# Optimization experiments

Hardware: AMD Instinct MI355X
Metric: run time of the kernel (lower is better)

Reference implementation:

```python
import jax, jax.numpy as jnp
import numpy as np

D_MODEL = 1024
NUM_HEADS = 16
D_K = D_MODEL // NUM_HEADS
LOCAL_WINDOW = 3
STRIDE = 4


def strided_mask(seq_len):
    # position i attends to j iff j <= i and (i-j <= local_window or (i-j) % stride == 0)
    i = jnp.arange(seq_len)[:, None]
    j = jnp.arange(seq_len)[None, :]
    d = i - j
    return (d >= 0) & ((d <= LOCAL_WINDOW) | (d % STRIDE == 0))


def setup_inputs() -> dict:
    key = jax.random.key(0)
    ks = jax.random.split(key, 11)
    B, S, D = 4, 1024, D_MODEL
    s = 1.0 / np.sqrt(D)
    inp = {
        "Q": jax.random.normal(ks[0], (B, S, D), jnp.float32),
        "K": jax.random.normal(ks[1], (B, S, D), jnp.float32),
        "V": jax.random.normal(ks[2], (B, S, D), jnp.float32),
        "Wq": jax.random.normal(ks[3], (D, D), jnp.float32) * s,
        "bq": jnp.zeros((D,), jnp.float32),
        "Wk": jax.random.normal(ks[4], (D, D), jnp.float32) * s,
        "bk": jnp.zeros((D,), jnp.float32),
        "Wv": jax.random.normal(ks[5], (D, D), jnp.float32) * s,
        "bv": jnp.zeros((D,), jnp.float32),
        "Wo": jax.random.normal(ks[6], (D, D), jnp.float32) * s,
        "bo": jnp.zeros((D,), jnp.float32),
    }
    return inp


def reference(Q, K, V, Wq, bq, Wk, bk, Wv, bv, Wo, bo):
    B, S, D = Q.shape
    H, dk = NUM_HEADS, D_K

    def split(x):  # [B,S,D] -> [B,H,S,dk]
        return x.reshape(B, S, H, dk).transpose(0, 2, 1, 3)

    q = split(Q @ Wq + bq)
    k = split(K @ Wk + bk)
    v = split(V @ Wv + bv)

    scores = jnp.einsum("bhsd,bhtd->bhst", q, k) / jnp.sqrt(
        jnp.asarray(dk, jnp.float32))
    m = strided_mask(S)[None, None]  # [1,1,S,S]
    scores = jnp.where(m, scores, -1e9)
    attn = jax.nn.softmax(scores, axis=-1)
    out = jnp.einsum("bhst,bhtd->bhsd", attn, v)
    out = out.transpose(0, 2, 1, 3).reshape(B, S, D)  # combine heads
    return out @ Wo + bo
```

## Files before the change

### kernel.cpp

```cpp
#include <hip/hip_runtime.h>

typedef _Float16 f16;
typedef __attribute__((ext_vector_type(8))) _Float16 f16x8;
typedef __attribute__((ext_vector_type(4))) _Float16 f16x4;
typedef __attribute__((ext_vector_type(4))) float f32x4;

#define MFMA16(a, b, c) __builtin_amdgcn_mfma_f32_16x16x32_f16((a), (b), (c), 0, 0, 0)

__device__ __forceinline__ void gld_lds16(const void* g, void* l) {
  __builtin_amdgcn_global_load_lds(
      (__attribute__((address_space(1))) void*)const_cast<void*>(g),
      (__attribute__((address_space(3))) void*)l, 16, 0, 0);
}

__device__ __forceinline__ f16x8 ld8(const f16* p) { return *(const f16x8*)p; }

__global__ __launch_bounds__(256) void prep_kernel(
    const float* __restrict__ Q, const float* __restrict__ K, const float* __restrict__ V,
    const float* __restrict__ Wq, const float* __restrict__ Wk,
    const float* __restrict__ Wv, const float* __restrict__ Wo,
    f16* __restrict__ Xq, f16* __restrict__ Xk, f16* __restrict__ Xv,
    f16* __restrict__ Tq, f16* __restrict__ Tk, f16* __restrict__ Tv, f16* __restrict__ To) {
  const int bx = blockIdx.x;
  __shared__ float tile[64][65];
  if (bx < 6144) {
    const int z = bx >> 11, blk = bx & 2047;
    const float* src = z == 0 ? Q : (z == 1 ? K : V);
    f16* dst = z == 0 ? Xq : (z == 1 ? Xk : Xv);
    size_t i = ((size_t)blk * 256 + threadIdx.x) * 8;
    float4 a = *(const float4*)(src + i);
    float4 b = *(const float4*)(src + i + 4);
    f16x8 h;
    h[0] = (f16)a.x; h[1] = (f16)a.y; h[2] = (f16)a.z; h[3] = (f16)a.w;
    h[4] = (f16)b.x; h[5] = (f16)b.y; h[6] = (f16)b.z; h[7] = (f16)b.w;
    *(f16x8*)(dst + i) = h;
  } else {
    const int idx = bx - 6144;
    const int z = idx >> 8, xy = idx & 255;
    const float* W = z == 0 ? Wq : (z == 1 ? Wk : (z == 2 ? Wv : Wo));
    f16* T = z == 0 ? Tq : (z == 1 ? Tk : (z == 2 ? Tv : To));
    const int k0 = (xy & 15) * 64, n0 = (xy >> 4) * 64;
    const int tx = threadIdx.x & 63, ty = threadIdx.x >> 6;
#pragma unroll
    for (int rr = 0; rr < 16; ++rr) {
      int r = rr * 4 + ty;
      tile[r][tx] = W[(size_t)(k0 + r) * 1024 + n0 + tx];
    }
    __syncthreads();
#pragma unroll
    for (int rr = 0; rr < 16; ++rr) {
      int nn = rr * 4 + ty;
      T[(size_t)(n0 + nn) * 1024 + k0 + tx] = (f16)tile[tx][nn];
    }
  }
}

__global__ __launch_bounds__(256) void gemm_qkv_kernel(
    const f16* __restrict__ Xq, const f16* __restrict__ Xk, const f16* __restrict__ Xv,
    const f16* __restrict__ Bq, const f16* __restrict__ Bk, const f16* __restrict__ Bv,
    const float* __restrict__ bq, const float* __restrict__ bk, const float* __restrict__ bv,
    f16* __restrict__ qh, f16* __restrict__ kh,
    f16* __restrict__ vh, f16* __restrict__ vtg) {
  const int z = blockIdx.z;
  const f16* A = z == 0 ? Xq : (z == 1 ? Xk : Xv);
  const f16* Bt = z == 0 ? Bq : (z == 1 ? Bk : Bv);
  const float* bias = z == 0 ? bq : (z == 1 ? bk : bv);

  __shared__ alignas(16) f16 lA[128 * 32];
  __shared__ alignas(16) f16 lB[128 * 32];

  const int t = threadIdx.x;
  const int w = t >> 6, lane = t & 63, quad = lane >> 4, l15 = lane & 15;
  const int wm = w >> 1, wn = w & 1;
  const int mbase = blockIdx.x * 128;
  const int nbase = blockIdx.y * 128;

  const f32x4 zero4 = {0.f, 0.f, 0.f, 0.f};
  f32x4 acc[4][4];
#pragma unroll
  for (int mi = 0; mi < 4; ++mi)
#pragma unroll
    for (int ni = 0; ni < 4; ++ni) acc[mi][ni] = zero4;

  const int r = t >> 2;
  const int koff = (t & 3) * 8;

  for (int k0 = 0; k0 < 1024; k0 += 32) {
    __syncthreads();
    gld_lds16(A + (size_t)(mbase + r) * 1024 + k0 + koff, (char*)lA + w * 1024);
    gld_lds16(A + (size_t)(mbase + 64 + r) * 1024 + k0 + koff, (char*)lA + 4096 + w * 1024);
    gld_lds16(Bt + (size_t)(nbase + r) * 1024 + k0 + koff, (char*)lB + w * 1024);
    gld_lds16(Bt + (size_t)(nbase + 64 + r) * 1024 + k0 + koff, (char*)lB + 4096 + w * 1024);
    __syncthreads();

    f16x8 af[4], bf[4];
#pragma unroll
    for (int mi = 0; mi < 4; ++mi)
      af[mi] = ld8(&lA[(wm * 64 + mi * 16 + l15) * 32 + quad * 8]);
#pragma unroll
    for (int ni = 0; ni < 4; ++ni)
      bf[ni] = ld8(&lB[(wn * 64 + ni * 16 + l15) * 32 + quad * 8]);
#pragma unroll
    for (int mi = 0; mi < 4; ++mi)
#pragma unroll
      for (int ni = 0; ni < 4; ++ni)
        acc[mi][ni] = MFMA16(af[mi], bf[ni], acc[mi][ni]);
  }

#pragma unroll
  for (int mi = 0; mi < 4; ++mi) {
#pragma unroll
    for (int ni = 0; ni < 4; ++ni) {
#pragma unroll
      for (int rg = 0; rg < 4; ++rg) {
        const int row = mbase + wm * 64 + mi * 16 + quad * 4 + rg;
        const int col = nbase + wn * 64 + ni * 16 + l15;
        const float v = acc[mi][ni][rg] + bias[col];
        const int bh = (row >> 10) * 16 + (col >> 6);
        const int s = row & 1023, d = col & 63;
        const f16 hv = (f16)v;
        if (z == 0) {
          qh[(size_t)bh * 65536 + s * 64 + d] = hv;
        } else if (z == 1) {
          kh[(size_t)bh * 65536 + s * 64 + d] = hv;
        } else {
          vh[(size_t)bh * 65536 + s * 64 + d] = hv;
          const int rr = s & 3, n = s >> 2, wi = n & 63;
          vtg[(size_t)bh * 65536 + (size_t)rr * 16384 + (size_t)d * 256 +
              (n & ~63) + ((wi & 15) << 2) + (wi >> 4)] = hv;
        }
      }
    }
  }
}

__global__ __launch_bounds__(256) void gemm_out_kernel(
    const f16* __restrict__ A, const f16* __restrict__ Bt,
    const float* __restrict__ bias, float* __restrict__ Cf) {
  __shared__ alignas(16) f16 lA[64 * 32];
  __shared__ alignas(16) f16 lB[128 * 32];

  const int t = threadIdx.x;
  const int w = t >> 6, lane = t & 63, quad = lane >> 4, l15 = lane & 15;
  const int wm = w >> 1, wn = w & 1;
  const int mbase = blockIdx.x * 64;
  const int nbase = blockIdx.y * 128;

  const f32x4 zero4 = {0.f, 0.f, 0.f, 0.f};
  f32x4 acc[2][4];
#pragma unroll
  for (int mi = 0; mi < 2; ++mi)
#pragma unroll
    for (int ni = 0; ni < 4; ++ni) acc[mi][ni] = zero4;

  const int r = t >> 2;
  const int koff = (t & 3) * 8;

  for (int k0 = 0; k0 < 1024; k0 += 32) {
    __syncthreads();
    gld_lds16(A + (size_t)(mbase + r) * 1024 + k0 + koff, (char*)lA + w * 1024);
    gld_lds16(Bt + (size_t)(nbase + r) * 1024 + k0 + koff, (char*)lB + w * 1024);
    gld_lds16(Bt + (size_t)(nbase + 64 + r) * 1024 + k0 + koff, (char*)lB + 4096 + w * 1024);
    __syncthreads();

    f16x8 af[2], bf[4];
#pragma unroll
    for (int mi = 0; mi < 2; ++mi)
      af[mi] = ld8(&lA[(wm * 32 + mi * 16 + l15) * 32 + quad * 8]);
#pragma unroll
    for (int ni = 0; ni < 4; ++ni)
      bf[ni] = ld8(&lB[(wn * 64 + ni * 16 + l15) * 32 + quad * 8]);
#pragma unroll
    for (int mi = 0; mi < 2; ++mi)
#pragma unroll
      for (int ni = 0; ni < 4; ++ni)
        acc[mi][ni] = MFMA16(af[mi], bf[ni], acc[mi][ni]);
  }

#pragma unroll
  for (int mi = 0; mi < 2; ++mi)
#pragma unroll
    for (int ni = 0; ni < 4; ++ni)
#pragma unroll
      for (int rg = 0; rg < 4; ++rg) {
        const int row = mbase + wm * 32 + mi * 16 + quad * 4 + rg;
        const int col = nbase + wn * 64 + ni * 16 + l15;
        Cf[(size_t)row * 1024 + col] = acc[mi][ni][rg] + bias[col];
      }
}

__global__ __launch_bounds__(256) void attn_far_kernel(
    const f16* __restrict__ qh, const f16* __restrict__ kh,
    const f16* __restrict__ vtg, float* __restrict__ po, float* __restrict__ ml) {
  const int t = threadIdx.x;
  const int w = t >> 6, lane = t & 63, quad = lane >> 4, l15 = lane & 15;
  const int widx = blockIdx.x + 512 * w;
  const int bh = (widx & 255) >> 2, r = widx & 3;
  const int wq = widx >> 8;
  const int m0 = wq * 32;
  const int ntiles = (wq >> 1) + 1;

  __shared__ alignas(16) f16 lp[4][2][16 * 72];

  const f16* qb = qh + (size_t)bh * 65536;
  const f16* kb = kh + (size_t)bh * 65536;
  const f16* vb = vtg + (size_t)bh * 65536 + (size_t)r * 16384;
  const float SCL2 = 0.125f * 1.44269504f;

  f16x8 aq[2][2];
#pragma unroll
  for (int mt = 0; mt < 2; ++mt) {
    const int i = 4 * (m0 + mt * 16 + l15) + r;
#pragma unroll
    for (int ko = 0; ko < 2; ++ko)
      aq[mt][ko] = ld8(qb + (size_t)i * 64 + ko * 32 + quad * 8);
  }

  const f32x4 zero4 = {0.f, 0.f, 0.f, 0.f};
  f32x4 o[2][4];
  float mrun[2][4], lrun[2][4];
#pragma unroll
  for (int mt = 0; mt < 2; ++mt)
#pragma unroll
    for (int i = 0; i < 4; ++i) {
      o[mt][i] = zero4; mrun[mt][i] = -1e30f; lrun[mt][i] = 0.f;
    }

  for (int jt = 0; jt < ntiles; ++jt) {
    const int n0 = jt * 64;
    f16x8 bk0[4], bk1[4], bv0[4], bv1[4];
#pragma unroll
    for (int nt = 0; nt < 4; ++nt) {
      const f16* kr = kb + (size_t)(4 * (n0 + nt * 16 + l15) + r) * 64;
      bk0[nt] = ld8(kr + quad * 8);
      bk1[nt] = ld8(kr + 32 + quad * 8);
      const f16* vr = vb + (size_t)(nt * 16 + l15) * 256 + n0;
      bv0[nt] = ld8(vr + quad * 8);
      bv1[nt] = ld8(vr + 32 + quad * 8);
    }
    const bool lastt = (jt == ntiles - 1);
#pragma unroll
    for (int mt = 0; mt < 2; ++mt) {
      f32x4 sc[4];
#pragma unroll
      for (int nt = 0; nt < 4; ++nt) {
        f32x4 c = MFMA16(aq[mt][0], bk0[nt], zero4);
        sc[nt] = MFMA16(aq[mt][1], bk1[nt], c);
      }
#pragma unroll
      for (int rg = 0; rg < 4; ++rg) {
        const int m = m0 + mt * 16 + quad * 4 + rg;
        float s[4];
#pragma unroll
        for (int nt = 0; nt < 4; ++nt) {
          float vsc = sc[nt][rg] * SCL2;
          if (lastt) vsc = (n0 + nt * 16 + l15 < m) ? vsc : -3.0e38f;
          s[nt] = vsc;
        }
        float tm = fmaxf(fmaxf(s[0], s[1]), fmaxf(s[2], s[3]));
        tm = fmaxf(tm, __shfl_xor(tm, 1));
        tm = fmaxf(tm, __shfl_xor(tm, 2));
        tm = fmaxf(tm, __shfl_xor(tm, 4));
        tm = fmaxf(tm, __shfl_xor(tm, 8));
        const float mnew = fmaxf(mrun[mt][rg], tm);
        const float alpha = exp2f(mrun[mt][rg] - mnew);
        float p[4], ps = 0.f;
#pragma unroll
        for (int nt = 0; nt < 4; ++nt) { p[nt] = exp2f(s[nt] - mnew); ps += p[nt]; }
        ps += __shfl_xor(ps, 1);
        ps += __shfl_xor(ps, 2);
        ps += __shfl_xor(ps, 4);
        ps += __shfl_xor(ps, 8);
        lrun[mt][rg] = lrun[mt][rg] * alpha + ps;
        mrun[mt][rg] = mnew;
#pragma unroll
        for (int ntv = 0; ntv < 4; ++ntv) o[mt][ntv][rg] *= alpha;
        f16x4 pk;
        pk.x = (f16)p[0]; pk.y = (f16)p[1]; pk.z = (f16)p[2]; pk.w = (f16)p[3];
        *(f16x4*)&lp[w][mt][(quad * 4 + rg) * 72 + l15 * 4] = pk;
      }
    }
#pragma unroll
    for (int mt = 0; mt < 2; ++mt) {
      const f16x8 ap0 = ld8(&lp[w][mt][l15 * 72 + quad * 8]);
      const f16x8 ap1 = ld8(&lp[w][mt][l15 * 72 + 32 + quad * 8]);
#pragma unroll
      for (int ntv = 0; ntv < 4; ++ntv) {
        f32x4 c = MFMA16(ap0, bv0[ntv], o[mt][ntv]);
        o[mt][ntv] = MFMA16(ap1, bv1[ntv], c);
      }
    }
  }

#pragma unroll
  for (int mt = 0; mt < 2; ++mt)
#pragma unroll
    for (int rg = 0; rg < 4; ++rg) {
      const int i = 4 * (m0 + mt * 16 + quad * 4 + rg) + r;
      const size_t idx = (size_t)bh * 1024 + i;
#pragma unroll
      for (int ntv = 0; ntv < 4; ++ntv)
        po[idx * 64 + ntv * 16 + l15] = o[mt][ntv][rg];
      if (l15 == 0) { ml[idx * 2] = mrun[mt][rg]; ml[idx * 2 + 1] = lrun[mt][rg]; }
    }
}

__global__ __launch_bounds__(256) void attn_diag_kernel(
    const f16* __restrict__ qh, const f16* __restrict__ kh, const f16* __restrict__ vh,
    const float* __restrict__ po, const float* __restrict__ ml, f16* __restrict__ ao) {
  const int t = threadIdx.x;
  const int widx = blockIdx.x * 4 + (t >> 6);
  const int l = t & 63;
  const int bh = widx >> 10, i = widx & 1023;
  const float SCL2 = 0.125f * 1.44269504f;

  const float q = (float)qh[(size_t)bh * 65536 + (size_t)i * 64 + l];
  float s[4];
#pragma unroll
  for (int d = 0; d < 4; ++d) {
    const int j = i - d;
    const int jc = j < 0 ? 0 : j;
    float pr = q * (float)kh[(size_t)bh * 65536 + (size_t)jc * 64 + l];
    pr += __shfl_xor(pr, 1);
    pr += __shfl_xor(pr, 2);
    pr += __shfl_xor(pr, 4);
    pr += __shfl_xor(pr, 8);
    pr += __shfl_xor(pr, 16);
    pr += __shfl_xor(pr, 32);
    s[d] = (j >= 0) ? pr * SCL2 : -3.0e38f;
  }
  const float md = fmaxf(fmaxf(s[0], s[1]), fmaxf(s[2], s[3]));
  const size_t idx = (size_t)bh * 1024 + i;
  const float mf = ml[idx * 2], lf = ml[idx * 2 + 1];
  const float M = fmaxf(md, mf);
  float p[4], ld = 0.f;
#pragma unroll
  for (int d = 0; d < 4; ++d) { p[d] = exp2f(s[d] - M); ld += p[d]; }
  float ov = 0.f;
#pragma unroll
  for (int d = 0; d < 4; ++d) {
    const int jc = (i - d) < 0 ? 0 : (i - d);
    ov += p[d] * (float)vh[(size_t)bh * 65536 + (size_t)jc * 64 + l];
  }
  const float fs = exp2f(mf - M);
  const float lt = lf * fs + ld;
  const float of = po[idx * 64 + l];
  const float res = (of * fs + ov) / lt;
  const int b = bh >> 4, h = bh & 15;
  ao[((size_t)(b * 1024 + i)) * 1024 + h * 64 + l] = (f16)res;
}

extern "C" void kernel_launch(void* const* d_in, const int* in_sizes, int n_in,
                              void* d_out, int out_size, void* d_ws, size_t ws_size,
                              hipStream_t stream) {
  const float* Q = (const float*)d_in[0];
  const float* K = (const float*)d_in[1];
  const float* V = (const float*)d_in[2];
  const float* Wq = (const float*)d_in[3];
  const float* bq = (const float*)d_in[4];
  const float* Wk = (const float*)d_in[5];
  const float* bk = (const float*)d_in[6];
  const float* Wv = (const float*)d_in[7];
  const float* bv = (const float*)d_in[8];
  const float* Wo = (const float*)d_in[9];
  const float* bo = (const float*)d_in[10];
  float* out = (float*)d_out;

  char* ws = (char*)d_ws;
  const size_t MB = 1ull << 20;
  f16* TWo = (f16*)(ws + 0 * MB);
  f16* TWq = (f16*)(ws + 2 * MB);
  f16* TWk = (f16*)(ws + 4 * MB);
  f16* TWv = (f16*)(ws + 6 * MB);
  f16* Xq  = (f16*)(ws + 8 * MB);
  f16* Xk  = (f16*)(ws + 16 * MB);
  f16* Xv  = (f16*)(ws + 24 * MB);
  f16* qhb = (f16*)(ws + 32 * MB);
  f16* khb = (f16*)(ws + 40 * MB);
  f16* vhb = (f16*)(ws + 48 * MB);
  f16* vtg = (f16*)(ws + 56 * MB);
  float* po  = (float*)(ws + 8 * MB);
  float* mlb = (float*)(ws + 24 * MB);
  f16* aob   = (f16*)(ws + 56 * MB);

  prep_kernel<<<dim3(7168), 256, 0, stream>>>(
      Q, K, V, Wq, Wk, Wv, Wo, Xq, Xk, Xv, TWq, TWk, TWv, TWo);
  gemm_qkv_kernel<<<dim3(32, 8, 3), 256, 0, stream>>>(
      Xq, Xk, Xv, TWq, TWk, TWv, bq, bk, bv, qhb, khb, vhb, vtg);
  attn_far_kernel<<<dim3(512), 256, 0, stream>>>(qhb, khb, vtg, po, mlb);
  attn_diag_kernel<<<dim3(16384), 256, 0, stream>>>(qhb, khb, vhb, po, mlb, aob);
  gemm_out_kernel<<<dim3(64, 8), 256, 0, stream>>>(aob, TWo, bo, out);
}
```

Baseline: 238.9 us.

## Fuse fp32-to-fp16 activation conversion into QKV GEMM and vectorize diag attention

Drops the separate pass that converted Q/K/V activations to fp16. The QKV GEMM now loads fp32 tiles directly into LDS and converts them to fp16 when building the MFMA operands, which saves a full read and write of the activations. The cost is twice the global-to-LDS traffic per A tile and a larger LDS footprint. The diagonal attention kernel is also reworked so each wave covers four diagonal offsets in parallel with 4-wide vector loads, cutting serial shuffle reductions. The workspace layout is rearranged to fit these changes.

```diff
diff --git a/kernel.cpp b/kernel.cpp
--- a/kernel.cpp
+++ b/kernel.cpp
@@ -15,58 +15,48 @@
 
 __device__ __forceinline__ f16x8 ld8(const f16* p) { return *(const f16x8*)p; }
 
-__global__ __launch_bounds__(256) void prep_kernel(
-    const float* __restrict__ Q, const float* __restrict__ K, const float* __restrict__ V,
+__device__ __forceinline__ f16x8 cvt8(const float4& a, const float4& b) {
+  f16x8 h;
+  h[0] = (f16)a.x; h[1] = (f16)a.y; h[2] = (f16)a.z; h[3] = (f16)a.w;
+  h[4] = (f16)b.x; h[5] = (f16)b.y; h[6] = (f16)b.z; h[7] = (f16)b.w;
+  return h;
+}
+
+__global__ __launch_bounds__(256) void cvt_wT_kernel(
     const float* __restrict__ Wq, const float* __restrict__ Wk,
     const float* __restrict__ Wv, const float* __restrict__ Wo,
-    f16* __restrict__ Xq, f16* __restrict__ Xk, f16* __restrict__ Xv,
     f16* __restrict__ Tq, f16* __restrict__ Tk, f16* __restrict__ Tv, f16* __restrict__ To) {
-  const int bx = blockIdx.x;
+  const int z = blockIdx.z;
+  const float* W = z == 0 ? Wq : (z == 1 ? Wk : (z == 2 ? Wv : Wo));
+  f16* T = z == 0 ? Tq : (z == 1 ? Tk : (z == 2 ? Tv : To));
   __shared__ float tile[64][65];
-  if (bx < 6144) {
-    const int z = bx >> 11, blk = bx & 2047;
-    const float* src = z == 0 ? Q : (z == 1 ? K : V);
-    f16* dst = z == 0 ? Xq : (z == 1 ? Xk : Xv);
-    size_t i = ((size_t)blk * 256 + threadIdx.x) * 8;
-    float4 a = *(const float4*)(src + i);
-    float4 b = *(const float4*)(src + i + 4);
-    f16x8 h;
-    h[0] = (f16)a.x; h[1] = (f16)a.y; h[2] = (f16)a.z; h[3] = (f16)a.w;
-    h[4] = (f16)b.x; h[5] = (f16)b.y; h[6] = (f16)b.z; h[7] = (f16)b.w;
-    *(f16x8*)(dst + i) = h;
-  } else {
-    const int idx = bx - 6144;
-    const int z = idx >> 8, xy = idx & 255;
-    const float* W = z == 0 ? Wq : (z == 1 ? Wk : (z == 2 ? Wv : Wo));
-    f16* T = z == 0 ? Tq : (z == 1 ? Tk : (z == 2 ? Tv : To));
-    const int k0 = (xy & 15) * 64, n0 = (xy >> 4) * 64;
-    const int tx = threadIdx.x & 63, ty = threadIdx.x >> 6;
-#pragma unroll
-    for (int rr = 0; rr < 16; ++rr) {
-      int r = rr * 4 + ty;
-      tile[r][tx] = W[(size_t)(k0 + r) * 1024 + n0 + tx];
-    }
-    __syncthreads();
-#pragma unroll
-    for (int rr = 0; rr < 16; ++rr) {
-      int nn = rr * 4 + ty;
-      T[(size_t)(n0 + nn) * 1024 + k0 + tx] = (f16)tile[tx][nn];
-    }
+  const int k0 = blockIdx.x * 64, n0 = blockIdx.y * 64;
+  const int tx = threadIdx.x & 63, ty = threadIdx.x >> 6;
+#pragma unroll
+  for (int rr = 0; rr < 16; ++rr) {
+    int r = rr * 4 + ty;
+    tile[r][tx] = W[(size_t)(k0 + r) * 1024 + n0 + tx];
+  }
+  __syncthreads();
+#pragma unroll
+  for (int rr = 0; rr < 16; ++rr) {
+    int nn = rr * 4 + ty;
+    T[(size_t)(n0 + nn) * 1024 + k0 + tx] = (f16)tile[tx][nn];
   }
 }
 
 __global__ __launch_bounds__(256) void gemm_qkv_kernel(
-    const f16* __restrict__ Xq, const f16* __restrict__ Xk, const f16* __restrict__ Xv,
+    const float* __restrict__ Q32, const float* __restrict__ K32, const float* __restrict__ V32,
     const f16* __restrict__ Bq, const f16* __restrict__ Bk, const f16* __restrict__ Bv,
     const float* __restrict__ bq, const float* __restrict__ bk, const float* __restrict__ bv,
     f16* __restrict__ qh, f16* __restrict__ kh,
     f16* __restrict__ vh, f16* __restrict__ vtg) {
   const int z = blockIdx.z;
-  const f16* A = z == 0 ? Xq : (z == 1 ? Xk : Xv);
+  const float* A32 = z == 0 ? Q32 : (z == 1 ? K32 : V32);
   const f16* Bt = z == 0 ? Bq : (z == 1 ? Bk : Bv);
   const float* bias = z == 0 ? bq : (z == 1 ? bk : bv);
 
-  __shared__ alignas(16) f16 lA[128 * 32];
+  __shared__ alignas(16) float lAf[128 * 32];
   __shared__ alignas(16) f16 lB[128 * 32];
 
   const int t = threadIdx.x;
@@ -84,19 +74,27 @@
 
   const int r = t >> 2;
   const int koff = (t & 3) * 8;
+  const int ra = t >> 3;
+  const int ca = (t & 7) * 4;
 
   for (int k0 = 0; k0 < 1024; k0 += 32) {
     __syncthreads();
-    gld_lds16(A + (size_t)(mbase + r) * 1024 + k0 + koff, (char*)lA + w * 1024);
-    gld_lds16(A + (size_t)(mbase + 64 + r) * 1024 + k0 + koff, (char*)lA + 4096 + w * 1024);
+#pragma unroll
+    for (int qq = 0; qq < 4; ++qq)
+      gld_lds16(A32 + (size_t)(mbase + qq * 32 + ra) * 1024 + k0 + ca,
+                (char*)lAf + qq * 4096 + w * 1024);
     gld_lds16(Bt + (size_t)(nbase + r) * 1024 + k0 + koff, (char*)lB + w * 1024);
     gld_lds16(Bt + (size_t)(nbase + 64 + r) * 1024 + k0 + koff, (char*)lB + 4096 + w * 1024);
     __syncthreads();
 
     f16x8 af[4], bf[4];
 #pragma unroll
-    for (int mi = 0; mi < 4; ++mi)
-      af[mi] = ld8(&lA[(wm * 64 + mi * 16 + l15) * 32 + quad * 8]);
+    for (int mi = 0; mi < 4; ++mi) {
+      const int row = wm * 64 + mi * 16 + l15;
+      const float4 f0 = *(const float4*)&lAf[row * 32 + quad * 8];
+      const float4 f1 = *(const float4*)&lAf[row * 32 + quad * 8 + 4];
+      af[mi] = cvt8(f0, f1);
+    }
 #pragma unroll
     for (int ni = 0; ni < 4; ++ni)
       bf[ni] = ld8(&lB[(wn * 64 + ni * 16 + l15) * 32 + quad * 8]);
@@ -311,43 +309,53 @@
   const int t = threadIdx.x;
   const int widx = blockIdx.x * 4 + (t >> 6);
   const int l = t & 63;
+  const int d = l >> 4, seg = l & 15;
   const int bh = widx >> 10, i = widx & 1023;
   const float SCL2 = 0.125f * 1.44269504f;
 
-  const float q = (float)qh[(size_t)bh * 65536 + (size_t)i * 64 + l];
-  float s[4];
-#pragma unroll
-  for (int d = 0; d < 4; ++d) {
-    const int j = i - d;
-    const int jc = j < 0 ? 0 : j;
-    float pr = q * (float)kh[(size_t)bh * 65536 + (size_t)jc * 64 + l];
-    pr += __shfl_xor(pr, 1);
-    pr += __shfl_xor(pr, 2);
-    pr += __shfl_xor(pr, 4);
-    pr += __shfl_xor(pr, 8);
-    pr += __shfl_xor(pr, 16);
-    pr += __shfl_xor(pr, 32);
-    s[d] = (j >= 0) ? pr * SCL2 : -3.0e38f;
-  }
-  const float md = fmaxf(fmaxf(s[0], s[1]), fmaxf(s[2], s[3]));
+  const int j = i - d;
+  const int jc = j < 0 ? 0 : j;
+
+  const f16x4 q4 = *(const f16x4*)(qh + (size_t)bh * 65536 + (size_t)i * 64 + seg * 4);
+  const f16x4 k4 = *(const f16x4*)(kh + (size_t)bh * 65536 + (size_t)jc * 64 + seg * 4);
+  float s = (float)q4.x * (float)k4.x + (float)q4.y * (float)k4.y +
+            (float)q4.z * (float)k4.z + (float)q4.w * (float)k4.w;
+  s += __shfl_xor(s, 1);
+  s += __shfl_xor(s, 2);
+  s += __shfl_xor(s, 4);
+  s += __shfl_xor(s, 8);
+  s = (j >= 0) ? s * SCL2 : -3.0e38f;
+
+  float md = fmaxf(s, __shfl_xor(s, 16));
+  md = fmaxf(md, __shfl_xor(md, 32));
+
   const size_t idx = (size_t)bh * 1024 + i;
   const float mf = ml[idx * 2], lf = ml[idx * 2 + 1];
   const float M = fmaxf(md, mf);
-  float p[4], ld = 0.f;
-#pragma unroll
-  for (int d = 0; d < 4; ++d) { p[d] = exp2f(s[d] - M); ld += p[d]; }
-  float ov = 0.f;
-#pragma unroll
-  for (int d = 0; d < 4; ++d) {
-    const int jc = (i - d) < 0 ? 0 : (i - d);
-    ov += p[d] * (float)vh[(size_t)bh * 65536 + (size_t)jc * 64 + l];
-  }
+  const float p = exp2f(s - M);
+  float ld = p + __shfl_xor(p, 16);
+  ld += __shfl_xor(ld, 32);
+
+  const f16x4 v4 = *(const f16x4*)(vh + (size_t)bh * 65536 + (size_t)jc * 64 + seg * 4);
+  float c0 = p * (float)v4.x, c1 = p * (float)v4.y;
+  float c2 = p * (float)v4.z, c3 = p * (float)v4.w;
+  c0 += __shfl_xor(c0, 16); c1 += __shfl_xor(c1, 16);
+  c2 += __shfl_xor(c2, 16); c3 += __shfl_xor(c3, 16);
+  c0 += __shfl_xor(c0, 32); c1 += __shfl_xor(c1, 32);
+  c2 += __shfl_xor(c2, 32); c3 += __shfl_xor(c3, 32);
+
   const float fs = exp2f(mf - M);
   const float lt = lf * fs + ld;
-  const float of = po[idx * 64 + l];
-  const float res = (of * fs + ov) / lt;
-  const int b = bh >> 4, h = bh & 15;
-  ao[((size_t)(b * 1024 + i)) * 1024 + h * 64 + l] = (f16)res;
+  if (d == 0) {
+    const float4 of = *(const float4*)(po + idx * 64 + seg * 4);
+    f16x4 res;
+    res.x = (f16)((of.x * fs + c0) / lt);
+    res.y = (f16)((of.y * fs + c1) / lt);
+    res.z = (f16)((of.z * fs + c2) / lt);
+    res.w = (f16)((of.w * fs + c3) / lt);
+    const int b = bh >> 4, h = bh & 15;
+    *(f16x4*)(ao + ((size_t)(b * 1024 + i)) * 1024 + h * 64 + seg * 4) = res;
+  }
 }
 
 extern "C" void kernel_launch(void* const* d_in, const int* in_sizes, int n_in,
@@ -368,25 +376,21 @@
 
   char* ws = (char*)d_ws;
   const size_t MB = 1ull << 20;
-  f16* TWo = (f16*)(ws + 0 * MB);
-  f16* TWq = (f16*)(ws + 2 * MB);
-  f16* TWk = (f16*)(ws + 4 * MB);
-  f16* TWv = (f16*)(ws + 6 * MB);
-  f16* Xq  = (f16*)(ws + 8 * MB);
-  f16* Xk  = (f16*)(ws + 16 * MB);
-  f16* Xv  = (f16*)(ws + 24 * MB);
+  f16* TWq = (f16*)(ws + 24 * MB);
+  f16* TWk = (f16*)(ws + 26 * MB);
+  f16* TWv = (f16*)(ws + 28 * MB);
+  f16* TWo = (f16*)(ws + 30 * MB);
   f16* qhb = (f16*)(ws + 32 * MB);
   f16* khb = (f16*)(ws + 40 * MB);
   f16* vhb = (f16*)(ws + 48 * MB);
   f16* vtg = (f16*)(ws + 56 * MB);
-  float* po  = (float*)(ws + 8 * MB);
-  float* mlb = (float*)(ws + 24 * MB);
-  f16* aob   = (f16*)(ws + 56 * MB);
-
-  prep_kernel<<<dim3(7168), 256, 0, stream>>>(
-      Q, K, V, Wq, Wk, Wv, Wo, Xq, Xk, Xv, TWq, TWk, TWv, TWo);
+  float* po  = (float*)(ws + 0 * MB);
+  float* mlb = (float*)(ws + 16 * MB);
+  f16* aob   = (f16*)(ws + 17 * MB);
+
+  cvt_wT_kernel<<<dim3(16, 16, 4), 256, 0, stream>>>(Wq, Wk, Wv, Wo, TWq, TWk, TWv, TWo);
   gemm_qkv_kernel<<<dim3(32, 8, 3), 256, 0, stream>>>(
-      Xq, Xk, Xv, TWq, TWk, TWv, bq, bk, bv, qhb, khb, vhb, vtg);
+      Q, K, V, TWq, TWk, TWv, bq, bk, bv, qhb, khb, vhb, vtg);
   attn_far_kernel<<<dim3(512), 256, 0, stream>>>(qhb, khb, vtg, po, mlb);
   attn_diag_kernel<<<dim3(16384), 256, 0, stream>>>(qhb, khb, vhb, po, mlb, aob);
   gemm_out_kernel<<<dim3(64, 8), 256, 0, stream>>>(aob, TWo, bo, out);
```

New measurement: 345.6 us. +44.7%, slower.
